# Kernel optimization log

Measured on AMD Instinct MI355X. Metric: run time of the kernel, lower is better.

Reference implementation:

```python
import jax, jax.numpy as jnp
import numpy as np

D_MODEL = 1024
N_HEADS = 16
D_K = D_MODEL // N_HEADS
NEG = -1e9


def setup_inputs() -> dict:
    key = jax.random.key(0)
    ks = jax.random.split(key, 6)
    B, T, D = 4, 2048, D_MODEL
    s = 1.0 / np.sqrt(D)
    x = jax.random.normal(ks[0], (B, T, D), dtype=jnp.float32)
    Wq = jax.random.normal(ks[1], (D, D), dtype=jnp.float32) * s
    Wk = jax.random.normal(ks[2], (D, D), dtype=jnp.float32) * s
    Wv = jax.random.normal(ks[3], (D, D), dtype=jnp.float32) * s
    Wo = jax.random.normal(ks[4], (D, D), dtype=jnp.float32) * s
    bo = jnp.zeros((D,), dtype=jnp.float32)
    # causal mask: True above diagonal = masked (masked_fill where True)
    mask = jnp.triu(jnp.ones((T, T), dtype=bool), k=1)
    return {"x": x, "mask": mask, "Wq": Wq, "Wk": Wk, "Wv": Wv, "Wo": Wo, "bo": bo}


def reference(x, mask, Wq, Wk, Wv, Wo, bo):
    B, T, D = x.shape
    # torch nn.Linear: y = x @ W.T
    q = (x @ Wq.T).reshape(B, T, N_HEADS, D_K).transpose(0, 2, 1, 3)  # [B,H,T,dk]
    k = (x @ Wk.T).reshape(B, T, N_HEADS, D_K).transpose(0, 2, 1, 3)
    v = (x @ Wv.T).reshape(B, T, N_HEADS, D_K).transpose(0, 2, 1, 3)
    scores = jnp.einsum("bhqd,bhkd->bhqk", q, k) / np.sqrt(D_K)  # [B,H,T,T]
    scores = jnp.where(mask[:T, :T], NEG, scores)
    attn = jax.nn.softmax(scores, axis=-1)
    ctx = jnp.einsum("bhqk,bhkd->bhqd", attn, v)  # [B,H,T,dk]
    ctx = ctx.transpose(0, 2, 1, 3).reshape(B, T, D)
    return ctx @ Wo.T + bo
```

## Files before the change

### kernel.cpp

```cpp
#include <hip/hip_runtime.h>
#include <hip/hip_bf16.h>


typedef __attribute__((ext_vector_type(8))) short bf16x8;
typedef __attribute__((ext_vector_type(4))) float f32x4;

__device__ __forceinline__ unsigned short f2b(float x) {
  __hip_bfloat16 h = __float2bfloat16(x);
  return __builtin_bit_cast(unsigned short, h);
}

__device__ __forceinline__ void load_lds16(const void* g, void* l) {
  __builtin_amdgcn_global_load_lds((__attribute__((address_space(1))) void*)g,
                                   (__attribute__((address_space(3))) void*)l,
                                   16, 0, 0);
}

__global__ void cast_kernel(const float* __restrict__ x,
                            const float* __restrict__ w0, const float* __restrict__ w1,
                            const float* __restrict__ w2, const float* __restrict__ w3,
                            unsigned short* __restrict__ xb, unsigned short* __restrict__ wb) {
  int i = blockIdx.x * 256 + threadIdx.x;
  const float* src;
  unsigned short* dst;
  int c;
  if (i < 1048576) {
    src = x; dst = xb; c = i;
  } else {
    int cw = i - 1048576;
    int wi = cw >> 17;
    c = cw & 131071;
    src = (wi == 0) ? w0 : (wi == 1) ? w1 : (wi == 2) ? w2 : w3;
    dst = wb + ((size_t)wi << 20);
  }
  const float4* s4 = (const float4*)src;
  float4 a = s4[2 * c], b = s4[2 * c + 1];
  union { unsigned short u[8]; uint4 v; } r;
  r.u[0] = f2b(a.x); r.u[1] = f2b(a.y); r.u[2] = f2b(a.z); r.u[3] = f2b(a.w);
  r.u[4] = f2b(b.x); r.u[5] = f2b(b.y); r.u[6] = f2b(b.z); r.u[7] = f2b(b.w);
  ((uint4*)dst)[c] = r.v;
}

__launch_bounds__(512, 2)
__global__ void gemm_qkv(const unsigned short* __restrict__ A,
                         const unsigned short* __restrict__ Bw,
                         unsigned short* __restrict__ Cout) {
  __shared__ unsigned short At[3][256 * 64];
  __shared__ unsigned short Bt[3][128 * 64];

  const int tid = threadIdx.x;
  const int lane = tid & 63;
  const int w = tid >> 6;
  const int quad = lane >> 4;
  const int l15 = lane & 15;
  const int m0 = blockIdx.x * 256;
  const int n0 = blockIdx.y * 128;
  const int wm = (w & 3) * 64;
  const int wn = (w >> 2) * 64;

  auto stageA = [&](int buf, int kt, int c) {
    int chunk = c * 512 + tid;
    int row = chunk >> 3;
    int scol = (chunk & 7) ^ (row & 7);
    load_lds16(A + (size_t)(m0 + row) * 1024 + kt + scol * 8,
               &At[buf][(c * 512 + (w << 6)) << 3]);
  };
  auto stageB = [&](int buf, int kt, int c) {
    int chunk = c * 512 + tid;
    int row = chunk >> 3;
    int scol = (chunk & 7) ^ (row & 7);
    load_lds16(Bw + (size_t)(n0 + row) * 1024 + kt + scol * 8,
               &Bt[buf][(c * 512 + (w << 6)) << 3]);
  };

  const f32x4 z4 = {0.f, 0.f, 0.f, 0.f};
  f32x4 acc[4][4];
#pragma unroll
  for (int i = 0; i < 4; ++i)
#pragma unroll
    for (int j = 0; j < 4; ++j) acc[i][j] = z4;

#pragma unroll
  for (int c = 0; c < 4; ++c) stageA(0, 0, c);
#pragma unroll
  for (int c = 0; c < 2; ++c) stageB(0, 0, c);
#pragma unroll
  for (int c = 0; c < 4; ++c) stageA(1, 64, c);
#pragma unroll
  for (int c = 0; c < 2; ++c) stageB(1, 64, c);
  asm volatile("s_waitcnt vmcnt(6)" ::: "memory");
  __builtin_amdgcn_s_barrier();
  __builtin_amdgcn_sched_barrier(0);

  int buf = 0;
  for (int t = 0; t < 16; ++t) {
    const int sbuf = (buf >= 1) ? buf - 1 : 2;
    const int skt = (t + 2) * 64;
    const bool st = (t < 14);

    bf16x8 bfv[4][2];
    bf16x8 afv[2][2];

#pragma unroll
    for (int j = 0; j < 4; ++j) {
      int rowB = wn + j * 16 + l15;
#pragma unroll
      for (int ks = 0; ks < 2; ++ks)
        bfv[j][ks] = *(const bf16x8*)&Bt[buf][rowB * 64 + (((ks * 4 + quad) ^ (rowB & 7)) << 3)];
    }
#pragma unroll
    for (int ii = 0; ii < 2; ++ii) {
      int rowA = wm + ii * 16 + l15;
#pragma unroll
      for (int ks = 0; ks < 2; ++ks)
        afv[ii][ks] = *(const bf16x8*)&At[buf][rowA * 64 + (((ks * 4 + quad) ^ (rowA & 7)) << 3)];
    }
    if (st) { stageA(sbuf, skt, 0); stageA(sbuf, skt, 1); stageB(sbuf, skt, 0); }
    __builtin_amdgcn_s_barrier();
    __builtin_amdgcn_sched_barrier(0);
    __builtin_amdgcn_s_setprio(1);
#pragma unroll
    for (int ii = 0; ii < 2; ++ii)
#pragma unroll
      for (int j = 0; j < 4; ++j)
#pragma unroll
        for (int ks = 0; ks < 2; ++ks)
          acc[ii][j] = __builtin_amdgcn_mfma_f32_16x16x32_bf16(afv[ii][ks], bfv[j][ks],
                                                               acc[ii][j], 0, 0, 0);
    __builtin_amdgcn_s_setprio(0);
    __builtin_amdgcn_s_barrier();
    __builtin_amdgcn_sched_barrier(0);

#pragma unroll
    for (int ii = 0; ii < 2; ++ii) {
      int rowA = wm + 32 + ii * 16 + l15;
#pragma unroll
      for (int ks = 0; ks < 2; ++ks)
        afv[ii][ks] = *(const bf16x8*)&At[buf][rowA * 64 + (((ks * 4 + quad) ^ (rowA & 7)) << 3)];
    }
    if (st) { stageA(sbuf, skt, 2); stageA(sbuf, skt, 3); stageB(sbuf, skt, 1); }
    __builtin_amdgcn_s_barrier();
    __builtin_amdgcn_sched_barrier(0);
    __builtin_amdgcn_s_setprio(1);
#pragma unroll
    for (int ii = 0; ii < 2; ++ii)
#pragma unroll
      for (int j = 0; j < 4; ++j)
#pragma unroll
        for (int ks = 0; ks < 2; ++ks)
          acc[2 + ii][j] = __builtin_amdgcn_mfma_f32_16x16x32_bf16(afv[ii][ks], bfv[j][ks],
                                                                   acc[2 + ii][j], 0, 0, 0);
    __builtin_amdgcn_s_setprio(0);

    if (t < 14) {
      asm volatile("s_waitcnt vmcnt(6)" ::: "memory");
    } else if (t == 14) {
      asm volatile("s_waitcnt vmcnt(0)" ::: "memory");
    }
    __builtin_amdgcn_s_barrier();
    __builtin_amdgcn_sched_barrier(0);

    buf = (buf < 2) ? buf + 1 : 0;
  }

  const int seg = n0 >> 10;
#pragma unroll
  for (int i = 0; i < 4; ++i) {
#pragma unroll
    for (int j = 0; j < 4; ++j) {
#pragma unroll
      for (int r = 0; r < 4; ++r) {
        int m = m0 + wm + i * 16 + quad * 4 + r;
        int n = n0 + wn + j * 16 + l15;
        int nn = n & 1023;
        float v = acc[i][j][r];
        if (seg == 0) {
          Cout[(size_t)m * 1024 + nn] = f2b(v);
        } else if (seg == 1) {
          (Cout + 8388608)[(size_t)m * 1024 + nn] = f2b(v);
        } else {
          int b = m >> 11, tq = m & 2047, hh = nn >> 6, d = nn & 63;
          (Cout + 16777216)[(((size_t)((b * 16 + hh) * 64 + d)) << 11) + tq] = f2b(v);
        }
      }
    }
  }
}

__launch_bounds__(256)
__global__ void gemm_proj(const unsigned short* __restrict__ A,
                          const unsigned short* __restrict__ Bw,
                          const float* __restrict__ bias,
                          float* __restrict__ out) {
  __shared__ unsigned short At[128 * 64];
  __shared__ unsigned short Bt[64 * 64];

  const int tid = threadIdx.x;
  const int lane = tid & 63;
  const int w = tid >> 6;
  const int quad = lane >> 4;
  const int l15 = lane & 15;
  const int m0 = blockIdx.x * 128;
  const int n0 = blockIdx.y * 64;
  const int wm = w * 32;

  const f32x4 z4 = {0.f, 0.f, 0.f, 0.f};
  f32x4 acc[2][4];
#pragma unroll
  for (int i = 0; i < 2; ++i)
#pragma unroll
    for (int j = 0; j < 4; ++j) acc[i][j] = z4;

  for (int kt = 0; kt < 1024; kt += 64) {
    __syncthreads();
#pragma unroll
    for (int c = 0; c < 4; ++c) {
      int chunk = c * 256 + tid;
      int row = chunk >> 3;
      int scol = (chunk & 7) ^ (row & 7);
      load_lds16(A + (size_t)(m0 + row) * 1024 + kt + scol * 8,
                 &At[((c * 256 + (w << 6)) << 3)]);
    }
#pragma unroll
    for (int c = 0; c < 2; ++c) {
      int chunk = c * 256 + tid;
      int row = chunk >> 3;
      int scol = (chunk & 7) ^ (row & 7);
      load_lds16(Bw + (size_t)(n0 + row) * 1024 + kt + scol * 8,
                 &Bt[((c * 256 + (w << 6)) << 3)]);
    }
    __syncthreads();
#pragma unroll
    for (int ks = 0; ks < 2; ++ks) {
      bf16x8 af[2], bf[4];
#pragma unroll
      for (int i = 0; i < 2; ++i) {
        int rowA = wm + i * 16 + l15;
        af[i] = *(const bf16x8*)&At[rowA * 64 + (((ks * 4 + quad) ^ (rowA & 7)) << 3)];
      }
#pragma unroll
      for (int j = 0; j < 4; ++j) {
        int rowB = j * 16 + l15;
        bf[j] = *(const bf16x8*)&Bt[rowB * 64 + (((ks * 4 + quad) ^ (rowB & 7)) << 3)];
      }
#pragma unroll
      for (int i = 0; i < 2; ++i)
#pragma unroll
        for (int j = 0; j < 4; ++j)
          acc[i][j] = __builtin_amdgcn_mfma_f32_16x16x32_bf16(af[i], bf[j], acc[i][j], 0, 0, 0);
    }
  }

#pragma unroll
  for (int i = 0; i < 2; ++i)
#pragma unroll
    for (int j = 0; j < 4; ++j) {
      int n = n0 + j * 16 + l15;
      float bv = bias[n];
#pragma unroll
      for (int r = 0; r < 4; ++r) {
        int m = m0 + wm + i * 16 + quad * 4 + r;
        out[(size_t)m * 1024 + n] = acc[i][j][r] + bv;
      }
    }
}

__launch_bounds__(256)
__global__ void attn_kernel(const unsigned short* __restrict__ Q,
                            const unsigned short* __restrict__ K,
                            const unsigned short* __restrict__ VT,
                            unsigned short* __restrict__ ctx) {
  __shared__ unsigned short Kt[2][64 * 64];
  __shared__ unsigned short Vt[2][64 * 64];
  __shared__ unsigned short Pt[64 * 64];

  const int tid = threadIdx.x;
  const int lane = tid & 63;
  const int w = tid >> 6;
  const int quad = lane >> 4;
  const int l15 = lane & 15;
  const int p = blockIdx.x;
  const int bh = blockIdx.y;
  const int b = bh >> 4, h = bh & 15;

  const unsigned short* Kg = K + ((size_t)(b * 2048)) * 1024 + h * 64;
  const unsigned short* Vg = VT + ((size_t)bh * 64) * 2048;

  const float SC = 0.1803368801f;
  const float M0 = 11.0f;

  for (int tt = 0; tt < 2; ++tt) {
    const int qt = tt ? (31 - p) : p;
    const int qb = qt * 64;

    const unsigned short* qbase =
        Q + ((size_t)(b * 2048 + qb + w * 16 + l15)) * 1024 + h * 64;
    bf16x8 qa[2];
    qa[0] = *(const bf16x8*)(qbase + quad * 8);
    qa[1] = *(const bf16x8*)(qbase + 32 + quad * 8);

    const f32x4 z4 = {0.f, 0.f, 0.f, 0.f};
    f32x4 o[4];
#pragma unroll
    for (int nt = 0; nt < 4; ++nt) o[nt] = z4;
    float lrow = 0.f;

    if (tt) __syncthreads();

#pragma unroll
    for (int c = 0; c < 2; ++c) {
      int chunk = c * 256 + tid;
      int row = chunk >> 3;
      int scol = (chunk & 7) ^ (row & 7);
      load_lds16(Kg + (size_t)row * 1024 + scol * 8, &Kt[0][((c * 256 + (w << 6)) << 3)]);
      load_lds16(Vg + ((size_t)row << 11) + scol * 8, &Vt[0][((c * 256 + (w << 6)) << 3)]);
    }

    int cur = 0;
    for (int j = 0; j <= qt; ++j) {
      const int j0 = j * 64;
      __syncthreads();

      if (j < qt) {
        const int nj0 = j0 + 64;
#pragma unroll
        for (int c = 0; c < 2; ++c) {
          int chunk = c * 256 + tid;
          int row = chunk >> 3;
          int scol = (chunk & 7) ^ (row & 7);
          load_lds16(Kg + (size_t)(nj0 + row) * 1024 + scol * 8,
                     &Kt[cur ^ 1][((c * 256 + (w << 6)) << 3)]);
          load_lds16(Vg + ((size_t)row << 11) + nj0 + scol * 8,
                     &Vt[cur ^ 1][((c * 256 + (w << 6)) << 3)]);
        }
      }

      f32x4 st[4];
#pragma unroll
      for (int nt = 0; nt < 4; ++nt) st[nt] = z4;
#pragma unroll
      for (int ks = 0; ks < 2; ++ks) {
#pragma unroll
        for (int nt = 0; nt < 4; ++nt) {
          int rowK = nt * 16 + l15;
          bf16x8 kf = *(const bf16x8*)&Kt[cur][rowK * 64 + (((ks * 4 + quad) ^ (rowK & 7)) << 3)];
          st[nt] = __builtin_amdgcn_mfma_f32_16x16x32_bf16(kf, qa[ks], st[nt], 0, 0, 0);
        }
      }

      const bool diag = (j == qt);
      const int q = qb + w * 16 + l15;
      float sum = 0.f;
#pragma unroll
      for (int nt = 0; nt < 4; ++nt) {
#pragma unroll
        for (int r = 0; r < 4; ++r) {
          float e = fmaf(st[nt][r], SC, -M0);
          if (diag) {
            int kpos = j0 + nt * 16 + quad * 4 + r;
            if (kpos > q) e = -1e30f;
          }
          float pv = exp2f(e);
          st[nt][r] = pv;
          sum += pv;
        }
      }
      sum += __shfl_xor(sum, 16);
      sum += __shfl_xor(sum, 32);
      lrow += sum;

      const int qrow = w * 16 + l15;
#pragma unroll
      for (int nt = 0; nt < 4; ++nt) {
        ushort4 pk;
        pk.x = f2b(st[nt][0]); pk.y = f2b(st[nt][1]);
        pk.z = f2b(st[nt][2]); pk.w = f2b(st[nt][3]);
        int chunk = nt * 4 + quad;
        *(ushort4*)&Pt[qrow * 64 + ((chunk ^ l15) << 2)] = pk;
      }

#pragma unroll
      for (int ks = 0; ks < 2; ++ks) {
        int c0 = ks * 8 + quad * 2;
        union { ushort4 hh[2]; bf16x8 v; } pu;
        pu.hh[0] = *(const ushort4*)&Pt[qrow * 64 + ((c0 ^ l15) << 2)];
        pu.hh[1] = *(const ushort4*)&Pt[qrow * 64 + (((c0 + 1) ^ l15) << 2)];
#pragma unroll
        for (int nt = 0; nt < 4; ++nt) {
          int rowV = nt * 16 + l15;
          bf16x8 vb = *(const bf16x8*)&Vt[cur][rowV * 64 + (((ks * 4 + quad) ^ (rowV & 7)) << 3)];
          o[nt] = __builtin_amdgcn_mfma_f32_16x16x32_bf16(pu.v, vb, o[nt], 0, 0, 0);
        }
      }
      cur ^= 1;
    }

    float lf[4];
#pragma unroll
    for (int r = 0; r < 4; ++r) lf[r] = 1.f / __shfl(lrow, quad * 4 + r);
#pragma unroll
    for (int nt = 0; nt < 4; ++nt) {
#pragma unroll
      for (int r = 0; r < 4; ++r) {
        int q = qb + w * 16 + quad * 4 + r;
        int dcol = nt * 16 + l15;
        ctx[((size_t)(b * 2048 + q)) * 1024 + h * 64 + dcol] = f2b(o[nt][r] * lf[r]);
      }
    }
  }
}

extern "C" void kernel_launch(void* const* d_in, const int* in_sizes, int n_in,
                              void* d_out, int out_size, void* d_ws, size_t ws_size,
                              hipStream_t stream) {
  const float* x  = (const float*)d_in[0];
  const float* Wq = (const float*)d_in[2];
  const float* Wk = (const float*)d_in[3];
  const float* Wv = (const float*)d_in[4];
  const float* Wo = (const float*)d_in[5];
  const float* bo = (const float*)d_in[6];
  float* out = (float*)d_out;

  unsigned short* xb  = (unsigned short*)d_ws;
  unsigned short* wb  = xb + 8388608;
  unsigned short* Qb  = wb + 4 * 1048576;
  unsigned short* Kb  = Qb + 8388608;
  unsigned short* VTb = Kb + 8388608;
  unsigned short* ctxb = xb;

  cast_kernel<<<6144, 256, 0, stream>>>(x, Wq, Wk, Wv, Wo, xb, wb);

  gemm_qkv<<<dim3(32, 24), 512, 0, stream>>>(xb, wb, Qb);

  attn_kernel<<<dim3(16, 64), 256, 0, stream>>>(Qb, Kb, VTb, ctxb);

  gemm_proj<<<dim3(64, 16), 256, 0, stream>>>(ctxb, wb + 3 * 1048576, bo, out);
}
```

Before: 295.2 us.

## Enlarge attention query tile to 128 rows per block for K/V reuse

Each wave now processes two 16-row query groups (128 query rows per block) and shares every K and V LDS fragment across both, so K/V tile loads and LDS reads per unit of work are halved. The grid is reshaped to 64x8 with bh on x, which changes block scheduling order, and the intrinsic exp2 replaces exp2f. In exchange there are more accumulator registers per thread, a larger P buffer in LDS, and half as many blocks, so occupancy and load balance may suffer. Causal masking is now applied per 16-row group against 64-wide K tiles.

```diff
diff --git a/kernel.cpp b/kernel.cpp
--- a/kernel.cpp
+++ b/kernel.cpp
@@ -272,15 +272,15 @@
                             unsigned short* __restrict__ ctx) {
   __shared__ unsigned short Kt[2][64 * 64];
   __shared__ unsigned short Vt[2][64 * 64];
-  __shared__ unsigned short Pt[64 * 64];
+  __shared__ unsigned short Pt[128 * 64];
 
   const int tid = threadIdx.x;
   const int lane = tid & 63;
   const int w = tid >> 6;
   const int quad = lane >> 4;
   const int l15 = lane & 15;
-  const int p = blockIdx.x;
-  const int bh = blockIdx.y;
+  const int bh = blockIdx.x;
+  const int pp = blockIdx.y;
   const int b = bh >> 4, h = bh & 15;
 
   const unsigned short* Kg = K + ((size_t)(b * 2048)) * 1024 + h * 64;
@@ -290,20 +290,26 @@
   const float M0 = 11.0f;
 
   for (int tt = 0; tt < 2; ++tt) {
-    const int qt = tt ? (31 - p) : p;
-    const int qb = qt * 64;
-
-    const unsigned short* qbase =
-        Q + ((size_t)(b * 2048 + qb + w * 16 + l15)) * 1024 + h * 64;
-    bf16x8 qa[2];
-    qa[0] = *(const bf16x8*)(qbase + quad * 8);
-    qa[1] = *(const bf16x8*)(qbase + 32 + quad * 8);
+    const int qt = tt ? (15 - pp) : pp;
+    const int qb = qt * 128;
+    const int jn = 2 * qt + 2;
+
+    bf16x8 qa[2][2];
+#pragma unroll
+    for (int g = 0; g < 2; ++g) {
+      const unsigned short* qbase =
+          Q + ((size_t)(b * 2048 + qb + w * 32 + g * 16 + l15)) * 1024 + h * 64;
+      qa[g][0] = *(const bf16x8*)(qbase + quad * 8);
+      qa[g][1] = *(const bf16x8*)(qbase + 32 + quad * 8);
+    }
 
     const f32x4 z4 = {0.f, 0.f, 0.f, 0.f};
-    f32x4 o[4];
-#pragma unroll
-    for (int nt = 0; nt < 4; ++nt) o[nt] = z4;
-    float lrow = 0.f;
+    f32x4 o[2][4];
+#pragma unroll
+    for (int g = 0; g < 2; ++g)
+#pragma unroll
+      for (int nt = 0; nt < 4; ++nt) o[g][nt] = z4;
+    float lrow[2] = {0.f, 0.f};
 
     if (tt) __syncthreads();
 
@@ -317,11 +323,11 @@
     }
 
     int cur = 0;
-    for (int j = 0; j <= qt; ++j) {
+    for (int j = 0; j < jn; ++j) {
       const int j0 = j * 64;
       __syncthreads();
 
-      if (j < qt) {
+      if (j + 1 < jn) {
         const int nj0 = j0 + 64;
 #pragma unroll
         for (int c = 0; c < 2; ++c) {
@@ -335,76 +341,94 @@
         }
       }
 
-      f32x4 st[4];
-#pragma unroll
-      for (int nt = 0; nt < 4; ++nt) st[nt] = z4;
+      f32x4 st[2][4];
+#pragma unroll
+      for (int g = 0; g < 2; ++g)
+#pragma unroll
+        for (int nt = 0; nt < 4; ++nt) st[g][nt] = z4;
 #pragma unroll
       for (int ks = 0; ks < 2; ++ks) {
 #pragma unroll
         for (int nt = 0; nt < 4; ++nt) {
           int rowK = nt * 16 + l15;
           bf16x8 kf = *(const bf16x8*)&Kt[cur][rowK * 64 + (((ks * 4 + quad) ^ (rowK & 7)) << 3)];
-          st[nt] = __builtin_amdgcn_mfma_f32_16x16x32_bf16(kf, qa[ks], st[nt], 0, 0, 0);
-        }
-      }
-
-      const bool diag = (j == qt);
-      const int q = qb + w * 16 + l15;
-      float sum = 0.f;
-#pragma unroll
-      for (int nt = 0; nt < 4; ++nt) {
-#pragma unroll
-        for (int r = 0; r < 4; ++r) {
-          float e = fmaf(st[nt][r], SC, -M0);
-          if (diag) {
-            int kpos = j0 + nt * 16 + quad * 4 + r;
-            if (kpos > q) e = -1e30f;
+          st[0][nt] = __builtin_amdgcn_mfma_f32_16x16x32_bf16(kf, qa[0][ks], st[0][nt], 0, 0, 0);
+          st[1][nt] = __builtin_amdgcn_mfma_f32_16x16x32_bf16(kf, qa[1][ks], st[1][nt], 0, 0, 0);
+        }
+      }
+
+#pragma unroll
+      for (int g = 0; g < 2; ++g) {
+        const int qmin = qb + w * 32 + g * 16;
+        const bool dg = (j0 + 63 > qmin);
+        const int q = qmin + l15;
+        float sum = 0.f;
+#pragma unroll
+        for (int nt = 0; nt < 4; ++nt) {
+#pragma unroll
+          for (int r = 0; r < 4; ++r) {
+            float e = fmaf(st[g][nt][r], SC, -M0);
+            if (dg) {
+              int kpos = j0 + nt * 16 + quad * 4 + r;
+              if (kpos > q) e = -1e30f;
+            }
+            float pv = __builtin_amdgcn_exp2f(e);
+            st[g][nt][r] = pv;
+            sum += pv;
           }
-          float pv = exp2f(e);
-          st[nt][r] = pv;
-          sum += pv;
-        }
-      }
-      sum += __shfl_xor(sum, 16);
-      sum += __shfl_xor(sum, 32);
-      lrow += sum;
-
-      const int qrow = w * 16 + l15;
-#pragma unroll
-      for (int nt = 0; nt < 4; ++nt) {
-        ushort4 pk;
-        pk.x = f2b(st[nt][0]); pk.y = f2b(st[nt][1]);
-        pk.z = f2b(st[nt][2]); pk.w = f2b(st[nt][3]);
-        int chunk = nt * 4 + quad;
-        *(ushort4*)&Pt[qrow * 64 + ((chunk ^ l15) << 2)] = pk;
+        }
+        sum += __shfl_xor(sum, 16);
+        sum += __shfl_xor(sum, 32);
+        lrow[g] += sum;
+      }
+
+#pragma unroll
+      for (int g = 0; g < 2; ++g) {
+        const int qrow = w * 32 + g * 16 + l15;
+#pragma unroll
+        for (int nt = 0; nt < 4; ++nt) {
+          ushort4 pk;
+          pk.x = f2b(st[g][nt][0]); pk.y = f2b(st[g][nt][1]);
+          pk.z = f2b(st[g][nt][2]); pk.w = f2b(st[g][nt][3]);
+          int chunk = nt * 4 + quad;
+          *(ushort4*)&Pt[qrow * 64 + ((chunk ^ l15) << 2)] = pk;
+        }
       }
 
 #pragma unroll
       for (int ks = 0; ks < 2; ++ks) {
         int c0 = ks * 8 + quad * 2;
-        union { ushort4 hh[2]; bf16x8 v; } pu;
-        pu.hh[0] = *(const ushort4*)&Pt[qrow * 64 + ((c0 ^ l15) << 2)];
-        pu.hh[1] = *(const ushort4*)&Pt[qrow * 64 + (((c0 + 1) ^ l15) << 2)];
+        union { ushort4 hh[2]; bf16x8 v; } pu[2];
+#pragma unroll
+        for (int g = 0; g < 2; ++g) {
+          const int qrow = w * 32 + g * 16 + l15;
+          pu[g].hh[0] = *(const ushort4*)&Pt[qrow * 64 + ((c0 ^ l15) << 2)];
+          pu[g].hh[1] = *(const ushort4*)&Pt[qrow * 64 + (((c0 + 1) ^ l15) << 2)];
+        }
 #pragma unroll
         for (int nt = 0; nt < 4; ++nt) {
           int rowV = nt * 16 + l15;
           bf16x8 vb = *(const bf16x8*)&Vt[cur][rowV * 64 + (((ks * 4 + quad) ^ (rowV & 7)) << 3)];
-          o[nt] = __builtin_amdgcn_mfma_f32_16x16x32_bf16(pu.v, vb, o[nt], 0, 0, 0);
+          o[0][nt] = __builtin_amdgcn_mfma_f32_16x16x32_bf16(pu[0].v, vb, o[0][nt], 0, 0, 0);
+          o[1][nt] = __builtin_amdgcn_mfma_f32_16x16x32_bf16(pu[1].v, vb, o[1][nt], 0, 0, 0);
         }
       }
       cur ^= 1;
     }
 
-    float lf[4];
-#pragma unroll
-    for (int r = 0; r < 4; ++r) lf[r] = 1.f / __shfl(lrow, quad * 4 + r);
-#pragma unroll
-    for (int nt = 0; nt < 4; ++nt) {
-#pragma unroll
-      for (int r = 0; r < 4; ++r) {
-        int q = qb + w * 16 + quad * 4 + r;
-        int dcol = nt * 16 + l15;
-        ctx[((size_t)(b * 2048 + q)) * 1024 + h * 64 + dcol] = f2b(o[nt][r] * lf[r]);
+#pragma unroll
+    for (int g = 0; g < 2; ++g) {
+      float lf[4];
+#pragma unroll
+      for (int r = 0; r < 4; ++r) lf[r] = 1.f / __shfl(lrow[g], quad * 4 + r);
+#pragma unroll
+      for (int nt = 0; nt < 4; ++nt) {
+#pragma unroll
+        for (int r = 0; r < 4; ++r) {
+          int q = qb + w * 32 + g * 16 + quad * 4 + r;
+          int dcol = nt * 16 + l15;
+          ctx[((size_t)(b * 2048 + q)) * 1024 + h * 64 + dcol] = f2b(o[g][nt][r] * lf[r]);
+        }
       }
     }
   }
@@ -432,7 +456,7 @@
 
   gemm_qkv<<<dim3(32, 24), 512, 0, stream>>>(xb, wb, Qb);
 
-  attn_kernel<<<dim3(16, 64), 256, 0, stream>>>(Qb, Kb, VTb, ctxb);
+  attn_kernel<<<dim3(64, 8), 256, 0, stream>>>(Qb, Kb, VTb, ctxb);
 
   gemm_proj<<<dim3(64, 16), 256, 0, stream>>>(ctxb, wb + 3 * 1048576, bo, out);
 }
```

Measured after the change: 278.7 us. -5.6%, faster.
